# Optimization experiments

Hardware: AMD Instinct MI355X
Metric: run time of the kernel (lower is better)

Reference implementation:

```python
import jax, jax.numpy as jnp
import numpy as np

T, B, D, H, L = 512, 512, 64, 128, 2
Y_LEN = 24


def gru_cell(x, h, Wih, Whh, bih, bhh):
    # PyTorch GRU cell, gate order (r, z, n)
    gi = x @ Wih.T + bih          # [B, 3H]
    gh = h @ Whh.T + bhh          # [B, 3H]
    ir, iz, i_n = jnp.split(gi, 3, axis=-1)
    hr, hz, h_n = jnp.split(gh, 3, axis=-1)
    r = jax.nn.sigmoid(ir + hr)
    z = jax.nn.sigmoid(iz + hz)
    n = jnp.tanh(i_n + r * h_n)
    return (1.0 - z) * n + z * h


def bigru_layer(inp, h0, Wih, Whh, bih, bhh):
    # inp [T,B,in]; Wih [2,3H,in]; Whh [2,3H,H]; bih/bhh [2,3H]; h0 [2,B,H]
    def step_f(h, x):
        h = gru_cell(x, h, Wih[0], Whh[0], bih[0], bhh[0])
        return h, h

    def step_b(h, x):
        h = gru_cell(x, h, Wih[1], Whh[1], bih[1], bhh[1])
        return h, h

    hf, out_f = jax.lax.scan(step_f, h0[0], inp)
    hb, out_b = jax.lax.scan(step_b, h0[1], jnp.flip(inp, 0))
    out_b = jnp.flip(out_b, 0)
    return jnp.concatenate([out_f, out_b], -1), hf, hb


def forward(x, enc_Wih0, enc_Wih1, enc_Whh, enc_bih, enc_bhh,
            dec_Wih0, dec_Wih1, dec_Whh, dec_bih, dec_bhh, fc_w, fc_b):
    batch = x.shape[1]
    # ---- encoder: 2-layer bidirectional GRU, h0 = 0 ----
    layer_in = x
    hn = []
    for l in range(L):
        Wih = enc_Wih0 if l == 0 else enc_Wih1
        h0 = jnp.zeros((2, batch, H), x.dtype)
        layer_in, hf, hb = bigru_layer(layer_in, h0, Wih, enc_Whh[l], enc_bih[l], enc_bhh[l])
        hn += [hf, hb]
    dec_h = jnp.stack(hn)                # [2L, B, H], layer-major (fwd, bwd)
    # dropout on h0 is eval-mode identity
    x0 = x[-1, :, 0:1]                   # [B, 1]

    def step(carry, _):
        xin, h = carry
        lin = xin
        new_h = []
        for l in range(L):
            Wih = dec_Wih0 if l == 0 else dec_Wih1
            hf = gru_cell(lin, h[2 * l],     Wih[0], dec_Whh[l, 0], dec_bih[l, 0], dec_bhh[l, 0])
            hb = gru_cell(lin, h[2 * l + 1], Wih[1], dec_Whh[l, 1], dec_bih[l, 1], dec_bhh[l, 1])
            lin = jnp.concatenate([hf, hb], -1)
            new_h += [hf, hb]
        pred = lin @ fc_w.T + fc_b       # [B, 1]
        return (pred, jnp.stack(new_h)), pred[:, 0]

    _, preds = jax.lax.scan(step, (x0, dec_h), None, length=Y_LEN)
    return preds[..., None]              # [24, B, 1]


def setup_inputs():
    key = jax.random.key(0)
    ks = jax.random.split(key, 13)
    scale = 1.0 / np.sqrt(H).astype(np.float32)
    u = lambda k, shape: jax.random.uniform(k, shape, jnp.float32, -scale, scale)
    return {
        "x": jax.random.normal(ks[0], (T, B, D), jnp.float32),
        "enc_Wih0": u(ks[1], (2, 3 * H, D)),
        "enc_Wih1": u(ks[2], (2, 3 * H, 2 * H)),
        "enc_Whh": u(ks[3], (L, 2, 3 * H, H)),
        "enc_bih": u(ks[4], (L, 2, 3 * H)),
        "enc_bhh": u(ks[5], (L, 2, 3 * H)),
        "dec_Wih0": u(ks[6], (2, 3 * H, 1)),
        "dec_Wih1": u(ks[7], (2, 3 * H, 2 * H)),
        "dec_Whh": u(ks[8], (L, 2, 3 * H, H)),
        "dec_bih": u(ks[9], (L, 2, 3 * H)),
        "dec_bhh": u(ks[10], (L, 2, 3 * H)),
        "fc_w": u(ks[11], (1, 2 * H)),
        "fc_b": u(ks[12], (1,)),
    }


def reference(x, enc_Wih0, enc_Wih1, enc_Whh, enc_bih, enc_bhh,
              dec_Wih0, dec_Wih1, dec_Whh, dec_bih, dec_bhh, fc_w, fc_b):
    return forward(x, enc_Wih0, enc_Wih1, enc_Whh, enc_bih, enc_bhh,
                   dec_Wih0, dec_Wih1, dec_Whh, dec_bih, dec_bhh, fc_w, fc_b)
```

## Files before the change

### kernel.cpp

```cpp
#include <hip/hip_runtime.h>
#include <cstdint>
#include <cstddef>


typedef __attribute__((ext_vector_type(8))) short short8_t;
typedef __attribute__((ext_vector_type(4))) short short4_t;
typedef __attribute__((ext_vector_type(4))) float f32x4_t;

#define MFMA16(a, b, c) __builtin_amdgcn_mfma_f32_16x16x32_bf16((a), (b), (c), 0, 0, 0)

static __device__ __forceinline__ float bf2f(unsigned short u) {
  unsigned int v = ((unsigned int)u) << 16;
  return __builtin_bit_cast(float, v);
}
static __device__ __forceinline__ unsigned short f2bf(float f) {
  unsigned int x = __builtin_bit_cast(unsigned int, f);
  x += 0x7fffu + ((x >> 16) & 1u);
  return (unsigned short)(x >> 16);
}
static __device__ __forceinline__ short8_t ld8(const unsigned short* p) {
  return *reinterpret_cast<const short8_t*>(p);
}
static __device__ __forceinline__ short8_t cvt8f(const float* p) {
  const f32x4_t* v = reinterpret_cast<const f32x4_t*>(p);
  f32x4_t a = v[0], b = v[1];
  short8_t r;
  r[0] = (short)f2bf(a[0]); r[1] = (short)f2bf(a[1]);
  r[2] = (short)f2bf(a[2]); r[3] = (short)f2bf(a[3]);
  r[4] = (short)f2bf(b[0]); r[5] = (short)f2bf(b[1]);
  r[6] = (short)f2bf(b[2]); r[7] = (short)f2bf(b[3]);
  return r;
}
static __device__ __forceinline__ float sigm(float x) { return 1.0f / (1.0f + __expf(-x)); }
static __device__ __forceinline__ float tanh_fast(float y) {
  float t = __expf(-2.0f * fabsf(y));
  float r = (1.0f - t) / (1.0f + t);
  return copysignf(r, y);
}

__global__ void k_prep(const float* __restrict__ x,
                       const float* __restrict__ dWih1, const float* __restrict__ dWhh,
                       unsigned short* __restrict__ bdWih1, unsigned short* __restrict__ bdWhh,
                       float* __restrict__ x0save) {
  const int NW = 24576;
  int i = blockIdx.x * blockDim.x + threadIdx.x;
  if (i < NW) {
    *reinterpret_cast<short8_t*>(bdWih1 + (size_t)i * 8) = cvt8f(dWih1 + (size_t)i * 8);
  } else if (i < 2 * NW) {
    int j = i - NW;
    *reinterpret_cast<short8_t*>(bdWhh + (size_t)j * 8) = cvt8f(dWhh + (size_t)j * 8);
  } else if (i < 2 * NW + 512) {
    int b = i - 2 * NW;
    x0save[b] = x[((size_t)511 * 512 + b) * 64];
  }
}

__global__ void k_copy(const float* __restrict__ x, float* __restrict__ xc,
                       int b_base, int Bc) {
  size_t i = (size_t)blockIdx.x * blockDim.x + threadIdx.x;
  size_t per = (size_t)Bc * 16;
  size_t n = (size_t)512 * per;
  if (i >= n) return;
  size_t t = i / per, r = i - t * per;
  const f32x4_t* s =
      reinterpret_cast<const f32x4_t*>(x + ((size_t)t * 512 + b_base) * 64) + r;
  f32x4_t* d = reinterpret_cast<f32x4_t*>(xc + t * per * 4) + r;
  *d = *s;
}

__global__ __launch_bounds__(256, 1) void k_scan0d(
    float* x,
    float* xc,
    const float* __restrict__ Wih,
    const float* __restrict__ bih,
    const float* __restrict__ Whh,
    const float* __restrict__ bhh,
    float* __restrict__ HS,
    int b_base, int Bc) {
  int dir = blockIdx.y;
  int bl0 = blockIdx.x * 16;
  int b0g = b_base + bl0;
  float* xin = dir ? xc : x;
  unsigned short* yout = (unsigned short*)xin;
  int xstr = dir ? Bc : 512;
  int xb0 = dir ? bl0 : b0g;
  int tid = threadIdx.x, w = tid >> 6, lane = tid & 63, q = lane >> 4, c16 = lane & 15;
  __shared__ unsigned short xl[2][16 * 72];
  __shared__ unsigned short hl[2][16 * 136];
  const float* Wi = Wih + (size_t)dir * 384 * 64;
  const float* Wh = Whh + (size_t)dir * 384 * 128;
  const float* bi = bih + dir * 384;
  const float* bh = bhh + dir * 384;

  short8_t fi[6][2], fh[6][4];
  float brz[4], bni[2], bnh[2];
#pragma unroll
  for (int g = 0; g < 3; g++)
#pragma unroll
    for (int cc = 0; cc < 2; cc++) {
      int f = g * 2 + cc;
      int n0 = g * 128 + w * 32 + cc * 16;
#pragma unroll
      for (int kt = 0; kt < 2; kt++)
        fi[f][kt] = cvt8f(Wi + (size_t)(n0 + c16) * 64 + kt * 32 + q * 8);
#pragma unroll
      for (int kt = 0; kt < 4; kt++)
        fh[f][kt] = cvt8f(Wh + (size_t)(n0 + c16) * 128 + kt * 32 + q * 8);
      if (g < 2) brz[f] = bi[n0 + c16] + bh[n0 + c16];
      else { bni[cc] = bi[n0 + c16]; bnh[cc] = bh[n0 + c16]; }
    }

  float h[2][4];
#pragma unroll
  for (int cc = 0; cc < 2; cc++)
#pragma unroll
    for (int rr = 0; rr < 4; rr++) h[cc][rr] = 0.f;
  for (int i = tid; i < 16 * 136; i += 256) hl[0][i] = 0;

  int srow = tid >> 4, sc = tid & 15;
  {
    int t0 = dir ? 511 : 0;
    f32x4_t v = *reinterpret_cast<const f32x4_t*>(
        xin + ((size_t)t0 * xstr + xb0 + srow) * 64 + sc * 4);
    unsigned short* dst = &xl[0][srow * 72 + sc * 4];
    dst[0] = f2bf(v[0]); dst[1] = f2bf(v[1]); dst[2] = f2bf(v[2]); dst[3] = f2bf(v[3]);
  }
  __syncthreads();

  for (int s = 0; s < 512; s++) {
    int cur = s & 1, nxt = cur ^ 1;
    if (s > 0) {
      int tp = dir ? (512 - s) : (s - 1);
      short8_t v = ld8(&hl[cur][srow * 136 + sc * 8]);
      *reinterpret_cast<short8_t*>(
          yout + ((size_t)tp * xstr + xb0 + srow) * 128 + sc * 8) = v;
    }
    f32x4_t xv;
    if (s < 511) {
      int tn = dir ? (510 - s) : (s + 1);
      xv = *reinterpret_cast<const f32x4_t*>(
          xin + ((size_t)tn * xstr + xb0 + srow) * 64 + sc * 4);
    }
    short8_t ax[2], ah[4];
#pragma unroll
    for (int kt = 0; kt < 2; kt++) ax[kt] = ld8(&xl[cur][c16 * 72 + kt * 32 + q * 8]);
#pragma unroll
    for (int kt = 0; kt < 4; kt++) ah[kt] = ld8(&hl[cur][c16 * 136 + kt * 32 + q * 8]);
    f32x4_t aRZ[4], aNi[2], aNh[2];
#pragma unroll
    for (int f = 0; f < 4; f++) aRZ[f] = (f32x4_t){0.f, 0.f, 0.f, 0.f};
#pragma unroll
    for (int cc = 0; cc < 2; cc++) {
      aNi[cc] = (f32x4_t){0.f, 0.f, 0.f, 0.f};
      aNh[cc] = (f32x4_t){0.f, 0.f, 0.f, 0.f};
    }
#pragma unroll
    for (int kt = 0; kt < 2; kt++) {
#pragma unroll
      for (int f = 0; f < 4; f++) aRZ[f] = MFMA16(ax[kt], fi[f][kt], aRZ[f]);
#pragma unroll
      for (int cc = 0; cc < 2; cc++) aNi[cc] = MFMA16(ax[kt], fi[4 + cc][kt], aNi[cc]);
    }
#pragma unroll
    for (int kt = 0; kt < 4; kt++) {
#pragma unroll
      for (int f = 0; f < 4; f++) aRZ[f] = MFMA16(ah[kt], fh[f][kt], aRZ[f]);
#pragma unroll
      for (int cc = 0; cc < 2; cc++) aNh[cc] = MFMA16(ah[kt], fh[4 + cc][kt], aNh[cc]);
    }
#pragma unroll
    for (int cc = 0; cc < 2; cc++)
#pragma unroll
      for (int rr = 0; rr < 4; rr++) {
        float r = sigm(aRZ[cc][rr] + brz[cc]);
        float z = sigm(aRZ[2 + cc][rr] + brz[2 + cc]);
        float n = tanh_fast(aNi[cc][rr] + bni[cc] + r * (aNh[cc][rr] + bnh[cc]));
        float hn = n + z * (h[cc][rr] - n);
        h[cc][rr] = hn;
        hl[nxt][(q * 4 + rr) * 136 + w * 32 + c16 + cc * 16] = f2bf(hn);
      }
    if (s < 511) {
      unsigned short* dst = &xl[nxt][srow * 72 + sc * 4];
      dst[0] = f2bf(xv[0]); dst[1] = f2bf(xv[1]); dst[2] = f2bf(xv[2]); dst[3] = f2bf(xv[3]);
    }
    __syncthreads();
  }
  {
    int tp = dir ? 0 : 511;
    short8_t v = ld8(&hl[0][srow * 136 + sc * 8]);
    *reinterpret_cast<short8_t*>(
        yout + ((size_t)tp * xstr + xb0 + srow) * 128 + sc * 8) = v;
  }
#pragma unroll
  for (int cc = 0; cc < 2; cc++)
#pragma unroll
    for (int rr = 0; rr < 4; rr++)
      HS[((size_t)dir * 512 + b0g + q * 4 + rr) * 128 + w * 32 + c16 + cc * 16] = h[cc][rr];
}

__global__ __launch_bounds__(512, 1) void k_scan1(
    const unsigned short* __restrict__ OutF,
    const unsigned short* __restrict__ OutB,
    const float* __restrict__ Wih1,
    const float* __restrict__ bih1,
    const float* __restrict__ Whh1,
    const float* __restrict__ bhh1,
    float* __restrict__ HS,
    int b_base, int Bc) {
  int dir = blockIdx.y;
  int b0l = blockIdx.x * 16;
  int tid = threadIdx.x, w = tid >> 6, lane = tid & 63, q = lane >> 4, c16 = lane & 15;
  __shared__ unsigned short il[2][16 * 264];
  __shared__ unsigned short hl[2][16 * 136];
  const float* Wi = Wih1 + (size_t)dir * 384 * 256;
  const float* Wh = Whh1 + (size_t)dir * 384 * 128;
  const float* bi = bih1 + dir * 384;
  const float* bh = bhh1 + dir * 384;

  short8_t fi[3][8], fh[3][4];
  float brz[2], bni, bnh;
#pragma unroll
  for (int g = 0; g < 3; g++) {
    int n0 = g * 128 + w * 16;
#pragma unroll
    for (int kt = 0; kt < 8; kt++)
      fi[g][kt] = cvt8f(Wi + (size_t)(n0 + c16) * 256 + kt * 32 + q * 8);
#pragma unroll
    for (int kt = 0; kt < 4; kt++)
      fh[g][kt] = cvt8f(Wh + (size_t)(n0 + c16) * 128 + kt * 32 + q * 8);
    if (g < 2) brz[g] = bi[n0 + c16] + bh[n0 + c16];
    else { bni = bi[n0 + c16]; bnh = bh[n0 + c16]; }
  }

  float h[4] = {0.f, 0.f, 0.f, 0.f};
  for (int i = tid; i < 16 * 136; i += 512) hl[0][i] = 0;

  int srow = tid >> 5, sc = tid & 31;
  {
    int t0 = dir ? 511 : 0;
    short8_t v = (sc < 16)
        ? ld8(OutF + ((size_t)t0 * 512 + b_base + b0l + srow) * 128 + sc * 8)
        : ld8(OutB + ((size_t)t0 * Bc + b0l + srow) * 128 + (sc - 16) * 8);
    *reinterpret_cast<short8_t*>(&il[0][srow * 264 + sc * 8]) = v;
  }
  __syncthreads();

  for (int s = 0; s < 512; s++) {
    int cur = s & 1, nxt = cur ^ 1;
    short8_t iv;
    if (s < 511) {
      int tn = dir ? (510 - s) : (s + 1);
      iv = (sc < 16)
          ? ld8(OutF + ((size_t)tn * 512 + b_base + b0l + srow) * 128 + sc * 8)
          : ld8(OutB + ((size_t)tn * Bc + b0l + srow) * 128 + (sc - 16) * 8);
    }
    f32x4_t aI[3], aH[3];
#pragma unroll
    for (int g = 0; g < 3; g++) {
      aI[g] = (f32x4_t){0.f, 0.f, 0.f, 0.f};
      aH[g] = (f32x4_t){0.f, 0.f, 0.f, 0.f};
    }
#pragma unroll
    for (int kt = 0; kt < 8; kt++) {
      short8_t a = ld8(&il[cur][c16 * 264 + kt * 32 + q * 8]);
#pragma unroll
      for (int g = 0; g < 3; g++) aI[g] = MFMA16(a, fi[g][kt], aI[g]);
    }
#pragma unroll
    for (int kt = 0; kt < 4; kt++) {
      short8_t a = ld8(&hl[cur][c16 * 136 + kt * 32 + q * 8]);
#pragma unroll
      for (int g = 0; g < 3; g++) aH[g] = MFMA16(a, fh[g][kt], aH[g]);
    }
#pragma unroll
    for (int rr = 0; rr < 4; rr++) {
      float r = sigm(aI[0][rr] + aH[0][rr] + brz[0]);
      float z = sigm(aI[1][rr] + aH[1][rr] + brz[1]);
      float n = tanh_fast(aI[2][rr] + bni + r * (aH[2][rr] + bnh));
      float hn = n + z * (h[rr] - n);
      h[rr] = hn;
      hl[nxt][(q * 4 + rr) * 136 + w * 16 + c16] = f2bf(hn);
    }
    if (s < 511)
      *reinterpret_cast<short8_t*>(&il[nxt][srow * 264 + sc * 8]) = iv;
    __syncthreads();
  }
#pragma unroll
  for (int rr = 0; rr < 4; rr++)
    HS[((size_t)(2 + dir) * 512 + b_base + b0l + q * 4 + rr) * 128 + w * 16 + c16] = h[rr];
}

__global__ __launch_bounds__(256, 1) void k_dec(
    const float* __restrict__ x0save,
    const float* __restrict__ HS,
    const unsigned short* __restrict__ Whh,
    const unsigned short* __restrict__ Wih1,
    const float* __restrict__ Wih0,
    const float* __restrict__ bih,
    const float* __restrict__ bhh,
    const float* __restrict__ fc_w,
    const float* __restrict__ fcb,
    float* __restrict__ out) {
  int b0 = blockIdx.x * 16;
  int tid = threadIdx.x, w = tid >> 6, lane = tid & 63, q = lane >> 4, c16 = lane & 15;
  __shared__ unsigned short hc0[16 * 264];
  __shared__ unsigned short hc1[16 * 264];
  __shared__ float x0s[16];
  __shared__ float fcwf[256];
  int jj = w * 32 + c16;
  int jw = w * 32;

  float hs[4][2][4];
#pragma unroll
  for (int cell = 0; cell < 4; cell++)
#pragma unroll
    for (int cc = 0; cc < 2; cc++)
#pragma unroll
      for (int rr = 0; rr < 4; rr++) {
        int row = q * 4 + rr, j = jj + cc * 16;
        float v = HS[((size_t)cell * 512 + b0 + row) * 128 + j];
        hs[cell][cc][rr] = v;
        unsigned short bv = f2bf(v);
        unsigned short* tile = (cell < 2) ? hc0 : hc1;
        tile[row * 264 + (cell & 1) * 128 + j] = bv;
      }
  if (tid < 16) x0s[tid] = x0save[b0 + tid];
  fcwf[tid] = fc_w[tid];

  float w0c[2][2][3], bi0[2][2][3], bh0[2][2][3], bi1[2][2][3], bh1[2][2][3];
#pragma unroll
  for (int d = 0; d < 2; d++)
#pragma unroll
    for (int cc = 0; cc < 2; cc++)
#pragma unroll
      for (int g = 0; g < 3; g++) {
        int col = g * 128 + jj + cc * 16;
        w0c[d][cc][g] = Wih0[d * 384 + col];
        bi0[d][cc][g] = bih[d * 384 + col];
        bh0[d][cc][g] = bhh[d * 384 + col];
        bi1[d][cc][g] = bih[(2 + d) * 384 + col];
        bh1[d][cc][g] = bhh[(2 + d) * 384 + col];
      }
  __syncthreads();

  for (int st = 0; st < 24; st++) {
    float hn0[2][2][4];
#pragma unroll
    for (int d = 0; d < 2; d++) {
      const unsigned short* Wd = Whh + (size_t)d * 384 * 128;
      short8_t a0[4];
#pragma unroll
      for (int kt = 0; kt < 4; kt++)
        a0[kt] = ld8(&hc0[c16 * 264 + d * 128 + kt * 32 + q * 8]);
      f32x4_t acc[6];
#pragma unroll
      for (int f = 0; f < 6; f++) acc[f] = (f32x4_t){0.f, 0.f, 0.f, 0.f};
#pragma unroll
      for (int kt = 0; kt < 4; kt++)
#pragma unroll
        for (int g = 0; g < 3; g++)
#pragma unroll
          for (int cc = 0; cc < 2; cc++) {
            int f = g * 2 + cc, n0 = g * 128 + jw + cc * 16;
            acc[f] = MFMA16(a0[kt], ld8(Wd + (size_t)(n0 + c16) * 128 + kt * 32 + q * 8), acc[f]);
          }
#pragma unroll
      for (int cc = 0; cc < 2; cc++)
#pragma unroll
        for (int rr = 0; rr < 4; rr++) {
          float xin = x0s[q * 4 + rr];
          float r = sigm(xin * w0c[d][cc][0] + bi0[d][cc][0] + acc[cc][rr] + bh0[d][cc][0]);
          float z = sigm(xin * w0c[d][cc][1] + bi0[d][cc][1] + acc[2 + cc][rr] + bh0[d][cc][1]);
          float n = tanh_fast(xin * w0c[d][cc][2] + bi0[d][cc][2] +
                              r * (acc[4 + cc][rr] + bh0[d][cc][2]));
          float hv = n + z * (hs[d][cc][rr] - n);
          hn0[d][cc][rr] = hv;
          hs[d][cc][rr] = hv;
        }
    }
    __syncthreads();
#pragma unroll
    for (int d = 0; d < 2; d++)
#pragma unroll
      for (int cc = 0; cc < 2; cc++)
#pragma unroll
        for (int rr = 0; rr < 4; rr++)
          hc0[(q * 4 + rr) * 264 + d * 128 + jj + cc * 16] = f2bf(hn0[d][cc][rr]);
    __syncthreads();

    short8_t ai[8];
#pragma unroll
    for (int kt = 0; kt < 8; kt++) ai[kt] = ld8(&hc0[c16 * 264 + kt * 32 + q * 8]);
    float hn1[2][2][4];
#pragma unroll
    for (int d = 0; d < 2; d++) {
      const unsigned short* Wh = Whh + (size_t)(2 + d) * 384 * 128;
      const unsigned short* Wi = Wih1 + (size_t)d * 384 * 256;
      short8_t ah[4];
#pragma unroll
      for (int kt = 0; kt < 4; kt++)
        ah[kt] = ld8(&hc1[c16 * 264 + d * 128 + kt * 32 + q * 8]);
      f32x4_t aRZ[4], aNi[2], aNh[2];
#pragma unroll
      for (int f = 0; f < 4; f++) aRZ[f] = (f32x4_t){0.f, 0.f, 0.f, 0.f};
#pragma unroll
      for (int cc = 0; cc < 2; cc++) {
        aNi[cc] = (f32x4_t){0.f, 0.f, 0.f, 0.f};
        aNh[cc] = (f32x4_t){0.f, 0.f, 0.f, 0.f};
      }
#pragma unroll
      for (int kt = 0; kt < 8; kt++) {
#pragma unroll
        for (int f = 0; f < 4; f++) {
          int n0 = (f >> 1) * 128 + jw + (f & 1) * 16;
          aRZ[f] = MFMA16(ai[kt], ld8(Wi + (size_t)(n0 + c16) * 256 + kt * 32 + q * 8), aRZ[f]);
        }
#pragma unroll
        for (int cc = 0; cc < 2; cc++) {
          int n0 = 256 + jw + cc * 16;
          aNi[cc] = MFMA16(ai[kt], ld8(Wi + (size_t)(n0 + c16) * 256 + kt * 32 + q * 8), aNi[cc]);
        }
      }
#pragma unroll
      for (int kt = 0; kt < 4; kt++) {
#pragma unroll
        for (int f = 0; f < 4; f++) {
          int n0 = (f >> 1) * 128 + jw + (f & 1) * 16;
          aRZ[f] = MFMA16(ah[kt], ld8(Wh + (size_t)(n0 + c16) * 128 + kt * 32 + q * 8), aRZ[f]);
        }
#pragma unroll
        for (int cc = 0; cc < 2; cc++) {
          int n0 = 256 + jw + cc * 16;
          aNh[cc] = MFMA16(ah[kt], ld8(Wh + (size_t)(n0 + c16) * 128 + kt * 32 + q * 8), aNh[cc]);
        }
      }
#pragma unroll
      for (int cc = 0; cc < 2; cc++)
#pragma unroll
        for (int rr = 0; rr < 4; rr++) {
          float r = sigm(aRZ[cc][rr] + bi1[d][cc][0] + bh1[d][cc][0]);
          float z = sigm(aRZ[2 + cc][rr] + bi1[d][cc][1] + bh1[d][cc][1]);
          float n = tanh_fast(aNi[cc][rr] + bi1[d][cc][2] + r * (aNh[cc][rr] + bh1[d][cc][2]));
          float hv = n + z * (hs[2 + d][cc][rr] - n);
          hn1[d][cc][rr] = hv;
          hs[2 + d][cc][rr] = hv;
        }
    }
    __syncthreads();
#pragma unroll
    for (int d = 0; d < 2; d++)
#pragma unroll
      for (int cc = 0; cc < 2; cc++)
#pragma unroll
        for (int rr = 0; rr < 4; rr++)
          hc1[(q * 4 + rr) * 264 + d * 128 + jj + cc * 16] = f2bf(hn1[d][cc][rr]);
    __syncthreads();

    if (w == 0) {
      float s = 0.f;
#pragma unroll
      for (int i = 0; i < 8; i++) {
        short8_t hv = ld8(&hc1[c16 * 264 + q * 64 + i * 8]);
#pragma unroll
        for (int e = 0; e < 8; e++)
          s += bf2f((unsigned short)hv[e]) * fcwf[q * 64 + i * 8 + e];
      }
      s += __shfl_xor(s, 16);
      s += __shfl_xor(s, 32);
      if (q == 0) {
        float pred = s + fcb[0];
        x0s[c16] = pred;
        out[(size_t)st * 512 + b0 + c16] = pred;
      }
    }
    __syncthreads();
  }
}

extern "C" void kernel_launch(void* const* d_in, const int* in_sizes, int n_in,
                              void* d_out, int out_size, void* d_ws, size_t ws_size,
                              hipStream_t stream) {
  const float* x     = (const float*)d_in[0];
  const float* eWih0 = (const float*)d_in[1];
  const float* eWih1 = (const float*)d_in[2];
  const float* eWhh  = (const float*)d_in[3];
  const float* ebih  = (const float*)d_in[4];
  const float* ebhh  = (const float*)d_in[5];
  const float* dWih0 = (const float*)d_in[6];
  const float* dWih1 = (const float*)d_in[7];
  const float* dWhh  = (const float*)d_in[8];
  const float* dbih  = (const float*)d_in[9];
  const float* dbhh  = (const float*)d_in[10];
  const float* fc_w  = (const float*)d_in[11];
  const float* fc_b  = (const float*)d_in[12];
  float* out = (float*)d_out;
  (void)in_sizes; (void)n_in; (void)out_size;

  const size_t fixedB = 2048 + 1048576 + 393216 + 393216 + 4096;
  int Bc = 256;
  if (fixedB + (size_t)512 * 131072 <= ws_size) Bc = 512;

  char* ws = (char*)d_ws;
  size_t off = 0;
  auto alloc = [&](size_t bytes) -> char* {
    off = (off + 255) & ~(size_t)255;
    char* p = ws + off;
    off += bytes;
    return p;
  };
  float* x0save          = (float*)alloc(2048);
  float* HS              = (float*)alloc(1048576);
  unsigned short* bdWih1 = (unsigned short*)alloc(393216);
  unsigned short* bdWhh  = (unsigned short*)alloc(393216);
  float* xc              = (float*)alloc((size_t)Bc * 131072);

  k_prep<<<194, 256, 0, stream>>>(x, dWih1, dWhh, bdWih1, bdWhh, x0save);

  float* xm = (float*)d_in[0];
  const float* Whh1 = eWhh + (size_t)2 * 384 * 128;
  int nchunks = 512 / Bc;
  for (int c = 0; c < nchunks; c++) {
    int b_base = c * Bc;
    int ncopy = (512 * Bc * 16 + 255) / 256;
    k_copy<<<ncopy, 256, 0, stream>>>(x, xc, b_base, Bc);
    k_scan0d<<<dim3(Bc / 16, 2), 256, 0, stream>>>(xm, xc, eWih0, ebih, eWhh, ebhh,
                                                   HS, b_base, Bc);
    k_scan1<<<dim3(Bc / 16, 2), 512, 0, stream>>>((const unsigned short*)xm,
                                                  (const unsigned short*)xc,
                                                  eWih1, ebih + 768, Whh1,
                                                  ebhh + 768, HS, b_base, Bc);
  }
  k_dec<<<dim3(32), 256, 0, stream>>>(x0save, HS, bdWhh, bdWih1, dWih0, dbih, dbhh,
                                      fc_w, fc_b, out);
}
```

Measured before the change: 2.157 ms.

## Load x fragments directly into registers and batch decoder weight loads

In the layer-0 encoder scan, the x tile no longer goes through shared memory. Each lane loads its MFMA A-fragment rows of x straight from global memory into registers, double-buffered across a 2x-unrolled loop, and packs them to bf16 just before use. In the decoder, the bf16 weight fragments are loaded into register arrays in batches ahead of the MFMA chains, so the loads can overlap instead of being interleaved one-by-one with the MFMAs. The cost is much higher register pressure (up to 72 short8 weight fragments live at once), which could cause spills, and each lane now issues redundant, less-coalesced global reads of x.

```diff
diff --git a/kernel.cpp b/kernel.cpp
--- a/kernel.cpp
+++ b/kernel.cpp
@@ -21,9 +21,20 @@
 static __device__ __forceinline__ short8_t ld8(const unsigned short* p) {
   return *reinterpret_cast<const short8_t*>(p);
 }
+static __device__ __forceinline__ f32x4_t ldf4(const float* p) {
+  return *reinterpret_cast<const f32x4_t*>(p);
+}
 static __device__ __forceinline__ short8_t cvt8f(const float* p) {
   const f32x4_t* v = reinterpret_cast<const f32x4_t*>(p);
   f32x4_t a = v[0], b = v[1];
+  short8_t r;
+  r[0] = (short)f2bf(a[0]); r[1] = (short)f2bf(a[1]);
+  r[2] = (short)f2bf(a[2]); r[3] = (short)f2bf(a[3]);
+  r[4] = (short)f2bf(b[0]); r[5] = (short)f2bf(b[1]);
+  r[6] = (short)f2bf(b[2]); r[7] = (short)f2bf(b[3]);
+  return r;
+}
+static __device__ __forceinline__ short8_t pack8(f32x4_t a, f32x4_t b) {
   short8_t r;
   r[0] = (short)f2bf(a[0]); r[1] = (short)f2bf(a[1]);
   r[2] = (short)f2bf(a[2]); r[3] = (short)f2bf(a[3]);
@@ -85,7 +96,6 @@
   int xstr = dir ? Bc : 512;
   int xb0 = dir ? bl0 : b0g;
   int tid = threadIdx.x, w = tid >> 6, lane = tid & 63, q = lane >> 4, c16 = lane & 15;
-  __shared__ unsigned short xl[2][16 * 72];
   __shared__ unsigned short hl[2][16 * 136];
   const float* Wi = Wih + (size_t)dir * 384 * 64;
   const float* Wh = Whh + (size_t)dir * 384 * 128;
@@ -118,16 +128,15 @@
   for (int i = tid; i < 16 * 136; i += 256) hl[0][i] = 0;
 
   int srow = tid >> 4, sc = tid & 15;
+  f32x4_t xaA[4], xaB[4];
   {
     int t0 = dir ? 511 : 0;
-    f32x4_t v = *reinterpret_cast<const f32x4_t*>(
-        xin + ((size_t)t0 * xstr + xb0 + srow) * 64 + sc * 4);
-    unsigned short* dst = &xl[0][srow * 72 + sc * 4];
-    dst[0] = f2bf(v[0]); dst[1] = f2bf(v[1]); dst[2] = f2bf(v[2]); dst[3] = f2bf(v[3]);
+    const float* p = xin + ((size_t)t0 * xstr + xb0 + c16) * 64 + q * 8;
+    xaA[0] = ldf4(p); xaA[1] = ldf4(p + 4); xaA[2] = ldf4(p + 32); xaA[3] = ldf4(p + 36);
   }
   __syncthreads();
 
-  for (int s = 0; s < 512; s++) {
+  auto body = [&](int s, const f32x4_t (&xu)[4], f32x4_t (&xnl)[4]) {
     int cur = s & 1, nxt = cur ^ 1;
     if (s > 0) {
       int tp = dir ? (512 - s) : (s - 1);
@@ -135,15 +144,15 @@
       *reinterpret_cast<short8_t*>(
           yout + ((size_t)tp * xstr + xb0 + srow) * 128 + sc * 8) = v;
     }
-    f32x4_t xv;
     if (s < 511) {
       int tn = dir ? (510 - s) : (s + 1);
-      xv = *reinterpret_cast<const f32x4_t*>(
-          xin + ((size_t)tn * xstr + xb0 + srow) * 64 + sc * 4);
-    }
-    short8_t ax[2], ah[4];
-#pragma unroll
-    for (int kt = 0; kt < 2; kt++) ax[kt] = ld8(&xl[cur][c16 * 72 + kt * 32 + q * 8]);
+      const float* p = xin + ((size_t)tn * xstr + xb0 + c16) * 64 + q * 8;
+      xnl[0] = ldf4(p); xnl[1] = ldf4(p + 4); xnl[2] = ldf4(p + 32); xnl[3] = ldf4(p + 36);
+    }
+    short8_t ax[2];
+    ax[0] = pack8(xu[0], xu[1]);
+    ax[1] = pack8(xu[2], xu[3]);
+    short8_t ah[4];
 #pragma unroll
     for (int kt = 0; kt < 4; kt++) ah[kt] = ld8(&hl[cur][c16 * 136 + kt * 32 + q * 8]);
     f32x4_t aRZ[4], aNi[2], aNh[2];
@@ -179,11 +188,12 @@
         h[cc][rr] = hn;
         hl[nxt][(q * 4 + rr) * 136 + w * 32 + c16 + cc * 16] = f2bf(hn);
       }
-    if (s < 511) {
-      unsigned short* dst = &xl[nxt][srow * 72 + sc * 4];
-      dst[0] = f2bf(xv[0]); dst[1] = f2bf(xv[1]); dst[2] = f2bf(xv[2]); dst[3] = f2bf(xv[3]);
-    }
-    __syncthreads();
+    __syncthreads();
+  };
+
+  for (int s2 = 0; s2 < 256; s2++) {
+    body(2 * s2, xaA, xaB);
+    body(2 * s2 + 1, xaB, xaA);
   }
   {
     int tp = dir ? 0 : 511;
@@ -352,6 +362,17 @@
 #pragma unroll
       for (int kt = 0; kt < 4; kt++)
         a0[kt] = ld8(&hc0[c16 * 264 + d * 128 + kt * 32 + q * 8]);
+      short8_t w0[24];
+#pragma unroll
+      for (int kt = 0; kt < 4; kt++)
+#pragma unroll
+        for (int g = 0; g < 3; g++)
+#pragma unroll
+          for (int cc = 0; cc < 2; cc++) {
+            int n0 = g * 128 + jw + cc * 16;
+            w0[kt * 6 + g * 2 + cc] =
+                ld8(Wd + (size_t)(n0 + c16) * 128 + kt * 32 + q * 8);
+          }
       f32x4_t acc[6];
 #pragma unroll
       for (int f = 0; f < 6; f++) acc[f] = (f32x4_t){0.f, 0.f, 0.f, 0.f};
@@ -361,8 +382,8 @@
         for (int g = 0; g < 3; g++)
 #pragma unroll
           for (int cc = 0; cc < 2; cc++) {
-            int f = g * 2 + cc, n0 = g * 128 + jw + cc * 16;
-            acc[f] = MFMA16(a0[kt], ld8(Wd + (size_t)(n0 + c16) * 128 + kt * 32 + q * 8), acc[f]);
+            int f = g * 2 + cc;
+            acc[f] = MFMA16(a0[kt], w0[kt * 6 + g * 2 + cc], acc[f]);
           }
 #pragma unroll
       for (int cc = 0; cc < 2; cc++)
@@ -400,6 +421,33 @@
 #pragma unroll
       for (int kt = 0; kt < 4; kt++)
         ah[kt] = ld8(&hc1[c16 * 264 + d * 128 + kt * 32 + q * 8]);
+      short8_t wA[24], wB[24], wH[24];
+#pragma unroll
+      for (int kt = 0; kt < 4; kt++) {
+#pragma unroll
+        for (int f = 0; f < 4; f++) {
+          int n0 = (f >> 1) * 128 + jw + (f & 1) * 16;
+          wA[kt * 6 + f] = ld8(Wi + (size_t)(n0 + c16) * 256 + kt * 32 + q * 8);
+        }
+#pragma unroll
+        for (int cc = 0; cc < 2; cc++) {
+          int n0 = 256 + jw + cc * 16;
+          wA[kt * 6 + 4 + cc] = ld8(Wi + (size_t)(n0 + c16) * 256 + kt * 32 + q * 8);
+        }
+      }
+#pragma unroll
+      for (int kt = 0; kt < 4; kt++) {
+#pragma unroll
+        for (int f = 0; f < 4; f++) {
+          int n0 = (f >> 1) * 128 + jw + (f & 1) * 16;
+          wB[kt * 6 + f] = ld8(Wi + (size_t)(n0 + c16) * 256 + (kt + 4) * 32 + q * 8);
+        }
+#pragma unroll
+        for (int cc = 0; cc < 2; cc++) {
+          int n0 = 256 + jw + cc * 16;
+          wB[kt * 6 + 4 + cc] = ld8(Wi + (size_t)(n0 + c16) * 256 + (kt + 4) * 32 + q * 8);
+        }
+      }
       f32x4_t aRZ[4], aNi[2], aNh[2];
 #pragma unroll
       for (int f = 0; f < 4; f++) aRZ[f] = (f32x4_t){0.f, 0.f, 0.f, 0.f};
@@ -409,30 +457,38 @@
         aNh[cc] = (f32x4_t){0.f, 0.f, 0.f, 0.f};
       }
 #pragma unroll
-      for (int kt = 0; kt < 8; kt++) {
+      for (int kt = 0; kt < 4; kt++) {
+#pragma unroll
+        for (int f = 0; f < 4; f++) aRZ[f] = MFMA16(ai[kt], wA[kt * 6 + f], aRZ[f]);
+#pragma unroll
+        for (int cc = 0; cc < 2; cc++) aNi[cc] = MFMA16(ai[kt], wA[kt * 6 + 4 + cc], aNi[cc]);
+      }
+#pragma unroll
+      for (int kt = 0; kt < 4; kt++) {
 #pragma unroll
         for (int f = 0; f < 4; f++) {
           int n0 = (f >> 1) * 128 + jw + (f & 1) * 16;
-          aRZ[f] = MFMA16(ai[kt], ld8(Wi + (size_t)(n0 + c16) * 256 + kt * 32 + q * 8), aRZ[f]);
+          wH[kt * 6 + f] = ld8(Wh + (size_t)(n0 + c16) * 128 + kt * 32 + q * 8);
         }
 #pragma unroll
         for (int cc = 0; cc < 2; cc++) {
           int n0 = 256 + jw + cc * 16;
-          aNi[cc] = MFMA16(ai[kt], ld8(Wi + (size_t)(n0 + c16) * 256 + kt * 32 + q * 8), aNi[cc]);
+          wH[kt * 6 + 4 + cc] = ld8(Wh + (size_t)(n0 + c16) * 128 + kt * 32 + q * 8);
         }
       }
 #pragma unroll
       for (int kt = 0; kt < 4; kt++) {
 #pragma unroll
-        for (int f = 0; f < 4; f++) {
-          int n0 = (f >> 1) * 128 + jw + (f & 1) * 16;
-          aRZ[f] = MFMA16(ah[kt], ld8(Wh + (size_t)(n0 + c16) * 128 + kt * 32 + q * 8), aRZ[f]);
-        }
-#pragma unroll
-        for (int cc = 0; cc < 2; cc++) {
-          int n0 = 256 + jw + cc * 16;
-          aNh[cc] = MFMA16(ah[kt], ld8(Wh + (size_t)(n0 + c16) * 128 + kt * 32 + q * 8), aNh[cc]);
-        }
+        for (int f = 0; f < 4; f++) aRZ[f] = MFMA16(ai[4 + kt], wB[kt * 6 + f], aRZ[f]);
+#pragma unroll
+        for (int cc = 0; cc < 2; cc++) aNi[cc] = MFMA16(ai[4 + kt], wB[kt * 6 + 4 + cc], aNi[cc]);
+      }
+#pragma unroll
+      for (int kt = 0; kt < 4; kt++) {
+#pragma unroll
+        for (int f = 0; f < 4; f++) aRZ[f] = MFMA16(ah[kt], wH[kt * 6 + f], aRZ[f]);
+#pragma unroll
+        for (int cc = 0; cc < 2; cc++) aNh[cc] = MFMA16(ah[kt], wH[kt * 6 + 4 + cc], aNh[cc]);
       }
 #pragma unroll
       for (int cc = 0; cc < 2; cc++)
```

After: 2.306 ms. +6.9%, slower.
